# Kernel tuning notes

Measured on AMD Instinct MI355X. Metric: run time of the kernel, lower is better.

## Reference

```python
import jax, jax.numpy as jnp
import numpy as np
from jax import lax

B, T, H, L, NV = 2048, 100, 256, 128, 5  # batch, max_len, hidden, latent, len(NUC_VOCAB)


def setup_inputs() -> dict:
    key = jax.random.key(0)
    ks = jax.random.split(key, 13)
    s = 0.05
    inp = {
        "x_seq": jax.random.uniform(ks[0], (B, T, NV), dtype=jnp.float32),
        "hidden_states": jax.random.normal(ks[1], (B, H), dtype=jnp.float32) * 0.1,
        "tree_latent_vec": jax.random.normal(ks[2], (B, L), dtype=jnp.float32),
        "graph_latent_vec": jax.random.normal(ks[3], (B, L), dtype=jnp.float32),
        "lengths": jnp.maximum(1, jax.random.randint(ks[4], (B,), 0, T + 1)).astype(jnp.int32),
        # concat_squash_linear: (H + L) -> H
        "W_cs": jax.random.normal(ks[5], (H + L, H), dtype=jnp.float32) * s,
        "b_cs": jnp.zeros((H,), dtype=jnp.float32),
        # GRU cell linears: (H + NV) -> H, acting on cat([x, h])
        "W_z": jax.random.normal(ks[6], (NV + H, H), dtype=jnp.float32) * s,
        "b_z": jnp.zeros((H,), dtype=jnp.float32),
        "W_r": jax.random.normal(ks[7], (NV + H, H), dtype=jnp.float32) * s,
        "b_r": jnp.zeros((H,), dtype=jnp.float32),
        "W_h": jax.random.normal(ks[8], (NV + H, H), dtype=jnp.float32) * s,
        "b_h": jnp.zeros((H,), dtype=jnp.float32),
    }
    return inp


def _decode(x_seq, hidden_states, tree_latent_vec, graph_latent_vec, lengths,
            W_cs, b_cs, W_z, b_z, W_r, b_r, W_h, b_h):
    # concat volatile hidden state with graph latent, squash back to H
    h0 = jax.nn.relu(jnp.concatenate([hidden_states, graph_latent_vec], axis=-1) @ W_cs + b_cs)

    def gru_step(h, x):  # h: [B,H], x: [B,NV]
        xh = jnp.concatenate([x, h], axis=-1)          # [B, NV+H]
        z = jax.nn.sigmoid(xh @ W_z + b_z)
        r = jax.nn.sigmoid(xh @ W_r + b_r)
        xg = jnp.concatenate([x, r * h], axis=-1)
        pre_h = jnp.tanh(xg @ W_h + b_h)
        new_h = (1.0 - z) * h + z * pre_h
        return new_h, new_h

    _, hs = lax.scan(gru_step, h0, jnp.swapaxes(x_seq, 0, 1))  # [T,B,H]
    all_h = jnp.swapaxes(hs, 0, 1)                              # [B,T,H]

    # gather hidden state at last valid timestep (pre_padding_idx)
    new_h = jnp.take_along_axis(all_h, (lengths - 1)[:, None, None], axis=1)[:, 0]  # [B,H]

    # per-segment max-pool over valid positions (segment_representation)
    mask = jnp.arange(T)[None, :] < lengths[:, None]            # [B,T]
    seg_rep = jnp.max(jnp.where(mask[:, :, None], all_h, -jnp.inf), axis=1)  # [B,H]

    # depadded token features concatenated with per-batch tree/graph latents;
    # kept padded [B,T,.] with zeros at invalid positions (fixed-shape form)
    tok = jnp.concatenate([
        all_h,
        jnp.broadcast_to(tree_latent_vec[:, None, :], (B, T, L)),
        jnp.broadcast_to(graph_latent_vec[:, None, :], (B, T, L)),
    ], axis=-1)                                                 # [B,T,H+2L]
    all_hidden_states = jnp.where(mask[:, :, None], tok, 0.0)
    return new_h, all_hidden_states, seg_rep


def reference(x_seq, hidden_states, tree_latent_vec, graph_latent_vec, lengths,
              W_cs, b_cs, W_z, b_z, W_r, b_r, W_h, b_h):
    return _decode(x_seq, hidden_states, tree_latent_vec, graph_latent_vec, lengths,
                   W_cs, b_cs, W_z, b_z, W_r, b_r, W_h, b_h)
```

## Files before the change

### kernel.cpp

```cpp
#include <hip/hip_runtime.h>
#include <stdint.h>

#define B_N 2048
#define T_N 100
#define H_N 256
#define L_N 128
#define NV_N 5
#define COLS 512

#define KCS 384
#define RB 8
#define NKQ 2
#define KQH 128
#define CH 16
#define NCH 8
#define HSTR 264

static constexpr int OUT_ALLH = B_N * H_N;
static constexpr int OUT_SEG  = OUT_ALLH + B_N * T_N * COLS;

__device__ __forceinline__ float bits2f(uint32_t u) {
    union { uint32_t u; float f; } v; v.u = u; return v.f;
}
__device__ __forceinline__ uint16_t f2bf(float f) {
    union { float f; uint32_t u; } v; v.f = f;
    uint32_t r = (v.u + 0x7FFFu + ((v.u >> 16) & 1u)) >> 16;
    return (uint16_t)r;
}

__device__ __forceinline__ int detect_f32(const uint32_t* __restrict__ w) {
    int cnt = 0;
    #pragma unroll 8
    for (int i = 0; i < 64; ++i) {
        uint32_t e = (w[i] >> 23) & 0xFFu;
        cnt += (e >= 97u && e <= 130u) ? 1 : 0;
    }
    return cnt >= 32 ? 1 : 0;
}

template <bool F32> struct IO;

template <> struct IO<true> {
    using Raw2 = float2;
    static __device__ __forceinline__ Raw2 ldraw2(const void* p, int idx) {
        return *(const float2*)((const float*)p + idx);
    }
    static __device__ __forceinline__ void cvt2(const Raw2& u, float f[2]) {
        f[0] = u.x; f[1] = u.y;
    }
    static __device__ __forceinline__ void ld4(const void* p, int idx, float f[4]) {
        const float4 v = *(const float4*)((const float*)p + idx);
        f[0] = v.x; f[1] = v.y; f[2] = v.z; f[3] = v.w;
    }
    static __device__ __forceinline__ float ld1(const void* p, int idx) {
        return ((const float*)p)[idx];
    }
    static __device__ __forceinline__ void st4(void* p, int idx, const float f[4]) {
        *(float4*)((float*)p + idx) = make_float4(f[0], f[1], f[2], f[3]);
    }
    static __device__ __forceinline__ void st4z(void* p, int idx) {
        *(float4*)((float*)p + idx) = make_float4(0.f, 0.f, 0.f, 0.f);
    }
};

template <> struct IO<false> {
    using Raw2 = uint32_t;
    static __device__ __forceinline__ Raw2 ldraw2(const void* p, int idx) {
        return *(const uint32_t*)((const uint16_t*)p + idx);
    }
    static __device__ __forceinline__ void cvt2(const Raw2& u, float f[2]) {
        f[0] = bits2f(u << 16);
        f[1] = bits2f(u & 0xFFFF0000u);
    }
    static __device__ __forceinline__ void ld4(const void* p, int idx, float f[4]) {
        uint2 u = *(const uint2*)((const uint16_t*)p + idx);
        f[0] = bits2f(u.x << 16);
        f[1] = bits2f(u.x & 0xFFFF0000u);
        f[2] = bits2f(u.y << 16);
        f[3] = bits2f(u.y & 0xFFFF0000u);
    }
    static __device__ __forceinline__ float ld1(const void* p, int idx) {
        return bits2f(((uint32_t)((const uint16_t*)p)[idx]) << 16);
    }
    static __device__ __forceinline__ void st4(void* p, int idx, const float f[4]) {
        uint2 u;
        u.x = (uint32_t)f2bf(f[0]) | ((uint32_t)f2bf(f[1]) << 16);
        u.y = (uint32_t)f2bf(f[2]) | ((uint32_t)f2bf(f[3]) << 16);
        *(uint2*)((uint16_t*)p + idx) = u;
    }
    static __device__ __forceinline__ void st4z(void* p, int idx) {
        *(uint2*)((uint16_t*)p + idx) = make_uint2(0u, 0u);
    }
};

__device__ __forceinline__ float sigmoid_f(float x) {
    x = fminf(fmaxf(x, -30.f), 30.f);
    return 1.f / (1.f + __expf(-x));
}
__device__ __forceinline__ float tanh_f(float x) {
    x = fminf(fmaxf(x, -15.f), 15.f);
    float e = __expf(-2.f * x);
    return (1.f - e) / (1.f + e);
}

template <bool F32>
__global__ __launch_bounds__(256) void latent_fill_kernel(
    const void* __restrict__ tree,
    const void* __restrict__ graph,
    const int* __restrict__ lengths,
    const void* __restrict__ Wcs_detect,
    void* __restrict__ out)
{
    __shared__ int s_is32;
    if (threadIdx.x == 0) s_is32 = detect_f32((const uint32_t*)Wcs_detect);
    __syncthreads();
    if ((s_is32 != 0) != F32) return;

    int idx = (int)(blockIdx.x * 256 + threadIdx.x);
    int c = (idx & 31) * 8;
    int bt = idx >> 5;
    int t = bt % T_N;
    int b = bt / T_N;

    int dst = OUT_ALLH + bt * COLS + H_N + c;
    if (t < lengths[b]) {
        float v[8];
        if (c < L_N) {
            IO<F32>::ld4(tree, b * L_N + c, v);
            IO<F32>::ld4(tree, b * L_N + c + 4, v + 4);
        } else {
            IO<F32>::ld4(graph, b * L_N + (c - L_N), v);
            IO<F32>::ld4(graph, b * L_N + (c - L_N) + 4, v + 4);
        }
        IO<F32>::st4(out, dst, v);
        IO<F32>::st4(out, dst + 4, v + 4);
    } else {
        IO<F32>::st4z(out, dst);
        IO<F32>::st4z(out, dst + 4);
    }
}

template <bool F32>
__global__ __launch_bounds__(256, 1) void gru_kernel(
    const void* __restrict__ x_seq,
    const void* __restrict__ hidden,
    const void* __restrict__ graph,
    const int* __restrict__ lengths,
    const void* __restrict__ Wcs, const void* __restrict__ bcs,
    const void* __restrict__ Wz,  const void* __restrict__ bz,
    const void* __restrict__ Wr,  const void* __restrict__ br,
    const void* __restrict__ Wh,  const void* __restrict__ bh,
    void* __restrict__ out)
{
    __shared__ float Pz[NKQ][RB][H_N];
    __shared__ float Pr[NKQ][RB][H_N];
    __shared__ float hstage[RB][HSTR];
    __shared__ float gstage[RB][HSTR];
    __shared__ int s_is32;
    __shared__ int s_len[RB];

    if (threadIdx.x == 0) s_is32 = detect_f32((const uint32_t*)Wcs);
    __syncthreads();
    if ((s_is32 != 0) != F32) return;

    const int tid = threadIdx.x;
    const int kq  = tid >> 7;
    const int c0  = (tid & 127) * 2;
    const int ro  = tid >> 5;
    const int c0g = (tid & 31) * 8;
    const int kh0 = kq * KQH;

    if (tid < RB) {
        int L = lengths[blockIdx.x * RB + tid];
        s_len[tid] = min(max(L, 1), T_N);
    }
    __syncthreads();

    const int b0  = blockIdx.x * RB;
    const int bo  = b0 + ro;
    const int len = s_len[ro];
    int maxlen = 1;
    #pragma unroll
    for (int i = 0; i < RB; ++i) maxlen = max(maxlen, s_len[i]);

    {
        float* cs = &Pz[0][0][0];
        for (int i = tid; i < RB * KCS; i += 256) {
            int r = i / KCS;
            int k = i - r * KCS;
            int bb = b0 + r;
            float v = (k < H_N) ? IO<F32>::ld1(hidden, bb * H_N + k)
                                : IO<F32>::ld1(graph,  bb * L_N + (k - H_N));
            cs[r * 388 + k] = v;
        }
    }
    __syncthreads();

    float h[8];
    {
        const float* cs = &Pz[0][0][0];
        float acc[8];
        IO<F32>::ld4(bcs, c0g, acc);
        IO<F32>::ld4(bcs, c0g + 4, acc + 4);
        for (int k = 0; k < KCS; k += 4) {
            const float4 hv = *reinterpret_cast<const float4*>(&cs[ro * 388 + k]);
            const float hvv[4] = {hv.x, hv.y, hv.z, hv.w};
            #pragma unroll
            for (int kk = 0; kk < 4; ++kk) {
                float w[8];
                IO<F32>::ld4(Wcs, (k + kk) * H_N + c0g, w);
                IO<F32>::ld4(Wcs, (k + kk) * H_N + c0g + 4, w + 4);
                #pragma unroll
                for (int j = 0; j < 8; ++j) acc[j] += hvv[kk] * w[j];
            }
        }
        #pragma unroll
        for (int j = 0; j < 8; ++j) h[j] = fmaxf(acc[j], 0.f);
    }

    float bzv[8], brv[8], bhv[8];
    IO<F32>::ld4(bz, c0g, bzv); IO<F32>::ld4(bz, c0g + 4, bzv + 4);
    IO<F32>::ld4(br, c0g, brv); IO<F32>::ld4(br, c0g + 4, brv + 4);
    IO<F32>::ld4(bh, c0g, bhv); IO<F32>::ld4(bh, c0g + 4, bhv + 4);

    float smax[8];
    #pragma unroll
    for (int j = 0; j < 8; ++j) smax[j] = -1e30f;

    __syncthreads();

    *reinterpret_cast<float4*>(&hstage[ro][c0g])     = make_float4(h[0], h[1], h[2], h[3]);
    *reinterpret_cast<float4*>(&hstage[ro][c0g + 4]) = make_float4(h[4], h[5], h[6], h[7]);

    const int xr = tid / NV_N;
    const int xi = tid - xr * NV_N;
    float xv = 0.f;
    if (tid < RB * NV_N) {
        float x0 = IO<F32>::ld1(x_seq, ((b0 + xr) * T_N + 0) * NV_N + xi);
        hstage[xr][H_N + xi] = x0;
        gstage[xr][H_N + xi] = x0;
        int tn = (1 < T_N) ? 1 : 0;
        xv = IO<F32>::ld1(x_seq, ((b0 + xr) * T_N + tn) * NV_N + xi);
    }
    __syncthreads();

    float z[8];

    typename IO<F32>::Raw2 zA[CH], rA[CH], zB[CH], rB[CH], hA[CH], hB[CH];
    typename IO<F32>::Raw2 xzb[NV_N], xrb[NV_N], xhb[NV_N];

#define P1_ISSUE(CHN, RZ, RR) { \
    const int kb_ = 5 + kh0 + (CHN) * CH; \
    _Pragma("unroll") \
    for (int i_ = 0; i_ < CH; ++i_) { \
        RZ[i_] = IO<F32>::ldraw2(Wz, (kb_ + i_) * H_N + c0); \
        RR[i_] = IO<F32>::ldraw2(Wr, (kb_ + i_) * H_N + c0); \
    } \
    __builtin_amdgcn_sched_barrier(0); }

#define P1_CONSUME(CHN, RZ, RR) { \
    const int kb_ = kh0 + (CHN) * CH; \
    _Pragma("unroll") \
    for (int g_ = 0; g_ < CH / 2; ++g_) { \
        float2 hr_[RB]; \
        _Pragma("unroll") \
        for (int r_ = 0; r_ < RB; ++r_) \
            hr_[r_] = *reinterpret_cast<const float2*>(&hstage[r_][kb_ + 2 * g_]); \
        _Pragma("unroll") \
        for (int u_ = 0; u_ < 2; ++u_) { \
            float wz2_[2], wr2_[2]; \
            IO<F32>::cvt2(RZ[2 * g_ + u_], wz2_); \
            IO<F32>::cvt2(RR[2 * g_ + u_], wr2_); \
            _Pragma("unroll") \
            for (int r_ = 0; r_ < RB; ++r_) { \
                const float hv_ = u_ ? hr_[r_].y : hr_[r_].x; \
                az[r_][0] += hv_ * wz2_[0]; \
                az[r_][1] += hv_ * wz2_[1]; \
                ar[r_][0] += hv_ * wr2_[0]; \
                ar[r_][1] += hv_ * wr2_[1]; \
            } } } }

#define P2_ISSUE(CHN, RH) { \
    const int kb_ = 5 + kh0 + (CHN) * CH; \
    _Pragma("unroll") \
    for (int i_ = 0; i_ < CH; ++i_) \
        RH[i_] = IO<F32>::ldraw2(Wh, (kb_ + i_) * H_N + c0); \
    __builtin_amdgcn_sched_barrier(0); }

#define P2_CONSUME(CHN, RH) { \
    const int kb_ = kh0 + (CHN) * CH; \
    _Pragma("unroll") \
    for (int g_ = 0; g_ < CH / 2; ++g_) { \
        float2 gr_[RB]; \
        _Pragma("unroll") \
        for (int r_ = 0; r_ < RB; ++r_) \
            gr_[r_] = *reinterpret_cast<const float2*>(&gstage[r_][kb_ + 2 * g_]); \
        _Pragma("unroll") \
        for (int u_ = 0; u_ < 2; ++u_) { \
            float wh2_[2]; \
            IO<F32>::cvt2(RH[2 * g_ + u_], wh2_); \
            _Pragma("unroll") \
            for (int r_ = 0; r_ < RB; ++r_) { \
                const float gv_ = u_ ? gr_[r_].y : gr_[r_].x; \
                ag[r_][0] += gv_ * wh2_[0]; \
                ag[r_][1] += gv_ * wh2_[1]; \
            } } } }

#define PX_ISSUE() if (kq == 0) { \
    _Pragma("unroll") \
    for (int i_ = 0; i_ < NV_N; ++i_) { \
        xzb[i_] = IO<F32>::ldraw2(Wz, i_ * H_N + c0); \
        xrb[i_] = IO<F32>::ldraw2(Wr, i_ * H_N + c0); \
    } }

#define PXH_ISSUE() if (kq == 0) { \
    _Pragma("unroll") \
    for (int i_ = 0; i_ < NV_N; ++i_) \
        xhb[i_] = IO<F32>::ldraw2(Wh, i_ * H_N + c0); }

#define P1X_CONSUME() if (kq == 0) { \
    _Pragma("unroll") \
    for (int i_ = 0; i_ < NV_N; ++i_) { \
        float wz2_[2], wr2_[2]; \
        IO<F32>::cvt2(xzb[i_], wz2_); \
        IO<F32>::cvt2(xrb[i_], wr2_); \
        _Pragma("unroll") \
        for (int r_ = 0; r_ < RB; ++r_) { \
            const float xv_ = hstage[r_][H_N + i_]; \
            az[r_][0] += xv_ * wz2_[0]; \
            az[r_][1] += xv_ * wz2_[1]; \
            ar[r_][0] += xv_ * wr2_[0]; \
            ar[r_][1] += xv_ * wr2_[1]; \
        } } }

#define P2X_CONSUME() if (kq == 0) { \
    _Pragma("unroll") \
    for (int i_ = 0; i_ < NV_N; ++i_) { \
        float wh2_[2]; \
        IO<F32>::cvt2(xhb[i_], wh2_); \
        _Pragma("unroll") \
        for (int r_ = 0; r_ < RB; ++r_) { \
            const float xv_ = gstage[r_][H_N + i_]; \
            ag[r_][0] += xv_ * wh2_[0]; \
            ag[r_][1] += xv_ * wh2_[1]; \
        } } }

    PX_ISSUE();
    P1_ISSUE(0, zA, rA);

    #pragma unroll 1
    for (int t = 0; t < maxlen; ++t) {
        float az[RB][2], ar[RB][2];
        #pragma unroll
        for (int r = 0; r < RB; ++r) {
            az[r][0] = 0.f; az[r][1] = 0.f;
            ar[r][0] = 0.f; ar[r][1] = 0.f;
        }
        #pragma unroll 1
        for (int ch = 0; ch < NCH; ch += 2) {
            P1_ISSUE(ch + 1, zB, rB);
            P1_CONSUME(ch, zA, rA);
            if (ch + 2 < NCH) { P1_ISSUE(ch + 2, zA, rA); }
            else              { P2_ISSUE(0, hA); PXH_ISSUE(); }
            P1_CONSUME(ch + 1, zB, rB);
        }
        P1X_CONSUME();
        #pragma unroll
        for (int r = 0; r < RB; ++r) {
            *reinterpret_cast<float2*>(&Pz[kq][r][c0]) = make_float2(az[r][0], az[r][1]);
            *reinterpret_cast<float2*>(&Pr[kq][r][c0]) = make_float2(ar[r][0], ar[r][1]);
        }
        __syncthreads();

        {
            float sz[8], sr[8];
            #pragma unroll
            for (int j = 0; j < 8; ++j) { sz[j] = bzv[j]; sr[j] = brv[j]; }
            #pragma unroll
            for (int q = 0; q < NKQ; ++q) {
                float4 a = *reinterpret_cast<const float4*>(&Pz[q][ro][c0g]);
                float4 b = *reinterpret_cast<const float4*>(&Pz[q][ro][c0g + 4]);
                sz[0] += a.x; sz[1] += a.y; sz[2] += a.z; sz[3] += a.w;
                sz[4] += b.x; sz[5] += b.y; sz[6] += b.z; sz[7] += b.w;
                a = *reinterpret_cast<const float4*>(&Pr[q][ro][c0g]);
                b = *reinterpret_cast<const float4*>(&Pr[q][ro][c0g + 4]);
                sr[0] += a.x; sr[1] += a.y; sr[2] += a.z; sr[3] += a.w;
                sr[4] += b.x; sr[5] += b.y; sr[6] += b.z; sr[7] += b.w;
            }
            float rh[8];
            #pragma unroll
            for (int j = 0; j < 8; ++j) {
                z[j] = sigmoid_f(sz[j]);
                rh[j] = sigmoid_f(sr[j]) * h[j];
            }
            *reinterpret_cast<float4*>(&gstage[ro][c0g])     = make_float4(rh[0], rh[1], rh[2], rh[3]);
            *reinterpret_cast<float4*>(&gstage[ro][c0g + 4]) = make_float4(rh[4], rh[5], rh[6], rh[7]);
        }
        __syncthreads();

        float ag[RB][2];
        #pragma unroll
        for (int r = 0; r < RB; ++r) { ag[r][0] = 0.f; ag[r][1] = 0.f; }
        #pragma unroll 1
        for (int ch = 0; ch < NCH; ch += 2) {
            P2_ISSUE(ch + 1, hB);
            P2_CONSUME(ch, hA);
            if (ch + 2 < NCH) { P2_ISSUE(ch + 2, hA); }
            else              { P1_ISSUE(0, zA, rA); PX_ISSUE(); }
            P2_CONSUME(ch + 1, hB);
        }
        P2X_CONSUME();
        #pragma unroll
        for (int r = 0; r < RB; ++r)
            *reinterpret_cast<float2*>(&Pz[kq][r][c0]) = make_float2(ag[r][0], ag[r][1]);
        __syncthreads();

        {
            float sg[8];
            #pragma unroll
            for (int j = 0; j < 8; ++j) sg[j] = bhv[j];
            #pragma unroll
            for (int q = 0; q < NKQ; ++q) {
                float4 a = *reinterpret_cast<const float4*>(&Pz[q][ro][c0g]);
                float4 b = *reinterpret_cast<const float4*>(&Pz[q][ro][c0g + 4]);
                sg[0] += a.x; sg[1] += a.y; sg[2] += a.z; sg[3] += a.w;
                sg[4] += b.x; sg[5] += b.y; sg[6] += b.z; sg[7] += b.w;
            }
            const bool active = (t < len);
            float hs[8];
            #pragma unroll
            for (int j = 0; j < 8; ++j) {
                float pre = tanh_f(sg[j]);
                float hn  = (1.f - z[j]) * h[j] + z[j] * pre;
                hn = active ? hn : h[j];
                h[j]  = hn;
                hs[j] = active ? hn : 0.f;
                smax[j] = active ? fmaxf(smax[j], hn) : smax[j];
            }
            const int ob = OUT_ALLH + (bo * T_N + t) * COLS + c0g;
            IO<F32>::st4(out, ob, hs);
            IO<F32>::st4(out, ob + 4, hs + 4);
            if (t == len - 1) {
                IO<F32>::st4(out, bo * H_N + c0g, h);
                IO<F32>::st4(out, bo * H_N + c0g + 4, h + 4);
            }
            *reinterpret_cast<float4*>(&hstage[ro][c0g])     = make_float4(h[0], h[1], h[2], h[3]);
            *reinterpret_cast<float4*>(&hstage[ro][c0g + 4]) = make_float4(h[4], h[5], h[6], h[7]);
        }
        if (tid < RB * NV_N) {
            hstage[xr][H_N + xi] = xv;
            gstage[xr][H_N + xi] = xv;
            int tn = (t + 2 < T_N) ? (t + 2) : (T_N - 1);
            xv = IO<F32>::ld1(x_seq, ((b0 + xr) * T_N + tn) * NV_N + xi);
        }
        __syncthreads();
    }

#undef P1_ISSUE
#undef P1_CONSUME
#undef P2_ISSUE
#undef P2_CONSUME
#undef PX_ISSUE
#undef PXH_ISSUE
#undef P1X_CONSUME
#undef P2X_CONSUME

    for (int t = maxlen; t < T_N; ++t) {
        const int ob = OUT_ALLH + (bo * T_N + t) * COLS + c0g;
        IO<F32>::st4z(out, ob);
        IO<F32>::st4z(out, ob + 4);
    }
    IO<F32>::st4(out, OUT_SEG + bo * H_N + c0g, smax);
    IO<F32>::st4(out, OUT_SEG + bo * H_N + c0g + 4, smax + 4);
}

extern "C" void kernel_launch(void* const* d_in, const int* in_sizes, int n_in,
                              void* d_out, int out_size, void* d_ws, size_t ws_size,
                              hipStream_t stream) {
    const void* x_seq  = d_in[0];
    const void* hidden = d_in[1];
    const void* tree   = d_in[2];
    const void* graph  = d_in[3];
    const int*  lens   = (const int*)d_in[4];
    const void* Wcs    = d_in[5];
    const void* bcs    = d_in[6];
    const void* Wz     = d_in[7];
    const void* bz     = d_in[8];
    const void* Wr     = d_in[9];
    const void* br     = d_in[10];
    const void* Wh     = d_in[11];
    const void* bh     = d_in[12];
    void* out = d_out;

    long long work = (long long)B_N * T_N * 32;
    int fill_blocks = (int)(work / 256);

    hipLaunchKernelGGL((latent_fill_kernel<true>),  dim3(fill_blocks), dim3(256), 0, stream,
                       tree, graph, lens, Wcs, out);
    hipLaunchKernelGGL((latent_fill_kernel<false>), dim3(fill_blocks), dim3(256), 0, stream,
                       tree, graph, lens, Wcs, out);

    hipLaunchKernelGGL((gru_kernel<true>), dim3(B_N / RB), dim3(256), 0, stream,
                       x_seq, hidden, graph, lens,
                       Wcs, bcs, Wz, bz, Wr, br, Wh, bh, out);
    hipLaunchKernelGGL((gru_kernel<false>), dim3(B_N / RB), dim3(256), 0, stream,
                       x_seq, hidden, graph, lens,
                       Wcs, bcs, Wz, bz, Wr, br, Wh, bh, out);
}
```

Baseline: 4.076 ms.

## Use bf16 MFMA with hi/lo split for GRU recurrence on bf16 inputs

New measurement: 4.107 ms. About the same (+0.8%).

```diff
diff --git a/kernel.cpp b/kernel.cpp
--- a/kernel.cpp
+++ b/kernel.cpp
@@ -10,6 +10,11 @@
 
 #define KCS 384
 #define RB 8
+
+#define KT_N 9
+#define PZ_STR 260
+#define HB_STR 296
+
 #define NKQ 2
 #define KQH 128
 #define CH 16
@@ -18,6 +23,10 @@
 
 static constexpr int OUT_ALLH = B_N * H_N;
 static constexpr int OUT_SEG  = OUT_ALLH + B_N * T_N * COLS;
+static constexpr size_t WS_NEEDED = (size_t)3 * KT_N * 16 * 64 * 8 * 2;
+
+typedef __attribute__((ext_vector_type(8))) short bf16x8v;
+typedef __attribute__((ext_vector_type(4))) float f32x4v;
 
 __device__ __forceinline__ float bits2f(uint32_t u) {
     union { uint32_t u; float f; } v; v.u = u; return v.f;
@@ -38,23 +47,36 @@
     return cnt >= 32 ? 1 : 0;
 }
 
+__device__ __forceinline__ float bld1(const void* p, int idx) {
+    return bits2f(((uint32_t)((const uint16_t*)p)[idx]) << 16);
+}
+__device__ __forceinline__ void bld4(const void* p, int idx, float f[4]) {
+    uint2 u = *(const uint2*)((const uint16_t*)p + idx);
+    f[0] = bits2f(u.x << 16); f[1] = bits2f(u.x & 0xFFFF0000u);
+    f[2] = bits2f(u.y << 16); f[3] = bits2f(u.y & 0xFFFF0000u);
+}
+__device__ __forceinline__ void bst4(void* p, int idx, const float f[4]) {
+    uint2 u;
+    u.x = (uint32_t)f2bf(f[0]) | ((uint32_t)f2bf(f[1]) << 16);
+    u.y = (uint32_t)f2bf(f[2]) | ((uint32_t)f2bf(f[3]) << 16);
+    *(uint2*)((uint16_t*)p + idx) = u;
+}
+__device__ __forceinline__ void bst4z(void* p, int idx) {
+    *(uint2*)((uint16_t*)p + idx) = make_uint2(0u, 0u);
+}
+
 template <bool F32> struct IO;
-
 template <> struct IO<true> {
     using Raw2 = float2;
     static __device__ __forceinline__ Raw2 ldraw2(const void* p, int idx) {
         return *(const float2*)((const float*)p + idx);
     }
-    static __device__ __forceinline__ void cvt2(const Raw2& u, float f[2]) {
-        f[0] = u.x; f[1] = u.y;
-    }
+    static __device__ __forceinline__ void cvt2(const Raw2& u, float f[2]) { f[0] = u.x; f[1] = u.y; }
     static __device__ __forceinline__ void ld4(const void* p, int idx, float f[4]) {
         const float4 v = *(const float4*)((const float*)p + idx);
         f[0] = v.x; f[1] = v.y; f[2] = v.z; f[3] = v.w;
     }
-    static __device__ __forceinline__ float ld1(const void* p, int idx) {
-        return ((const float*)p)[idx];
-    }
+    static __device__ __forceinline__ float ld1(const void* p, int idx) { return ((const float*)p)[idx]; }
     static __device__ __forceinline__ void st4(void* p, int idx, const float f[4]) {
         *(float4*)((float*)p + idx) = make_float4(f[0], f[1], f[2], f[3]);
     }
@@ -62,35 +84,18 @@
         *(float4*)((float*)p + idx) = make_float4(0.f, 0.f, 0.f, 0.f);
     }
 };
-
 template <> struct IO<false> {
     using Raw2 = uint32_t;
     static __device__ __forceinline__ Raw2 ldraw2(const void* p, int idx) {
         return *(const uint32_t*)((const uint16_t*)p + idx);
     }
     static __device__ __forceinline__ void cvt2(const Raw2& u, float f[2]) {
-        f[0] = bits2f(u << 16);
-        f[1] = bits2f(u & 0xFFFF0000u);
-    }
-    static __device__ __forceinline__ void ld4(const void* p, int idx, float f[4]) {
-        uint2 u = *(const uint2*)((const uint16_t*)p + idx);
-        f[0] = bits2f(u.x << 16);
-        f[1] = bits2f(u.x & 0xFFFF0000u);
-        f[2] = bits2f(u.y << 16);
-        f[3] = bits2f(u.y & 0xFFFF0000u);
-    }
-    static __device__ __forceinline__ float ld1(const void* p, int idx) {
-        return bits2f(((uint32_t)((const uint16_t*)p)[idx]) << 16);
-    }
-    static __device__ __forceinline__ void st4(void* p, int idx, const float f[4]) {
-        uint2 u;
-        u.x = (uint32_t)f2bf(f[0]) | ((uint32_t)f2bf(f[1]) << 16);
-        u.y = (uint32_t)f2bf(f[2]) | ((uint32_t)f2bf(f[3]) << 16);
-        *(uint2*)((uint16_t*)p + idx) = u;
-    }
-    static __device__ __forceinline__ void st4z(void* p, int idx) {
-        *(uint2*)((uint16_t*)p + idx) = make_uint2(0u, 0u);
-    }
+        f[0] = bits2f(u << 16); f[1] = bits2f(u & 0xFFFF0000u);
+    }
+    static __device__ __forceinline__ void ld4(const void* p, int idx, float f[4]) { bld4(p, idx, f); }
+    static __device__ __forceinline__ float ld1(const void* p, int idx) { return bld1(p, idx); }
+    static __device__ __forceinline__ void st4(void* p, int idx, const float f[4]) { bst4(p, idx, f); }
+    static __device__ __forceinline__ void st4z(void* p, int idx) { bst4z(p, idx); }
 };
 
 __device__ __forceinline__ float sigmoid_f(float x) {
@@ -138,6 +143,321 @@
         IO<F32>::st4z(out, dst);
         IO<F32>::st4z(out, dst + 4);
     }
+}
+
+__global__ __launch_bounds__(256) void prep_kernel(
+    const void* __restrict__ Wz, const void* __restrict__ Wr,
+    const void* __restrict__ Wh, const void* __restrict__ Wcs_detect,
+    void* __restrict__ ws)
+{
+    __shared__ int s_is32;
+    if (threadIdx.x == 0) s_is32 = detect_f32((const uint32_t*)Wcs_detect);
+    __syncthreads();
+    const int is32 = s_is32;
+
+    int g = (int)(blockIdx.x * 256 + threadIdx.x);
+    int lane  = g & 63;
+    int rest  = g >> 6;
+    int nt    = rest & 15;
+    int rest2 = rest >> 4;
+    int kt    = rest2 % KT_N;
+    int mat   = rest2 / KT_N;
+    if (mat > 2) return;
+
+    const void* W = (mat == 0) ? Wz : (mat == 1) ? Wr : Wh;
+    const int n = nt * 16 + (lane & 15);
+    uint16_t u[8];
+    #pragma unroll
+    for (int j = 0; j < 8; ++j) {
+        int k = kt * 32 + ((lane >> 4) * 8) + j;
+        int srow = (k < 256) ? (k + NV_N) : ((k <= 260) ? (k - 256) : -1);
+        uint16_t v = 0;
+        if (srow >= 0) {
+            if (is32) v = f2bf(((const float*)W)[srow * H_N + n]);
+            else      v = ((const uint16_t*)W)[srow * H_N + n];
+        }
+        u[j] = v;
+    }
+    uint4 o;
+    o.x = (uint32_t)u[0] | ((uint32_t)u[1] << 16);
+    o.y = (uint32_t)u[2] | ((uint32_t)u[3] << 16);
+    o.z = (uint32_t)u[4] | ((uint32_t)u[5] << 16);
+    o.w = (uint32_t)u[6] | ((uint32_t)u[7] << 16);
+    *(uint4*)((char*)ws + (size_t)g * 16) = o;
+}
+
+__global__ __launch_bounds__(256, 1) void gru_mfma(
+    const void* __restrict__ x_seq,
+    const void* __restrict__ hidden,
+    const void* __restrict__ graph,
+    const int* __restrict__ lengths,
+    const void* __restrict__ Wcs, const void* __restrict__ bcs,
+    const void* __restrict__ bz,  const void* __restrict__ br,
+    const void* __restrict__ bh,
+    const void* __restrict__ ws,  void* __restrict__ out)
+{
+    __shared__ float PzS[16 * PZ_STR];
+    __shared__ float PrS[16 * PZ_STR];
+    __shared__ uint16_t hbf[16 * HB_STR];
+    __shared__ uint16_t gbf[16 * HB_STR];
+    __shared__ int s_is32;
+    __shared__ int s_len[RB];
+
+    if (threadIdx.x == 0) s_is32 = detect_f32((const uint32_t*)Wcs);
+    __syncthreads();
+    if (s_is32 != 0) return;
+
+    const int tid  = threadIdx.x;
+    const int lane = tid & 63;
+    const int wv   = tid >> 6;
+    const int ntb  = wv * 4;
+    const int ro   = tid >> 5;
+    const int c0g  = (tid & 31) * 8;
+
+    if (tid < RB) {
+        int L = lengths[blockIdx.x * RB + tid];
+        s_len[tid] = min(max(L, 1), T_N);
+    }
+    for (int i = tid; i < 16 * HB_STR; i += 256) { hbf[i] = 0; gbf[i] = 0; }
+    __syncthreads();
+
+    const int b0  = blockIdx.x * RB;
+    const int bo  = b0 + ro;
+    const int len = s_len[ro];
+    int maxlen = 1;
+    #pragma unroll
+    for (int i = 0; i < RB; ++i) maxlen = max(maxlen, s_len[i]);
+
+    {
+        float* cs = PzS;
+        for (int i = tid; i < RB * KCS; i += 256) {
+            int r = i / KCS, k = i - r * KCS;
+            int bb = b0 + r;
+            float v = (k < H_N) ? bld1(hidden, bb * H_N + k)
+                                : bld1(graph,  bb * L_N + (k - H_N));
+            cs[r * 388 + k] = v;
+        }
+    }
+    __syncthreads();
+
+    float h[8];
+    {
+        const float* cs = PzS;
+        float acc[8];
+        bld4(bcs, c0g, acc); bld4(bcs, c0g + 4, acc + 4);
+        for (int k = 0; k < KCS; k += 4) {
+            const float4 hv = *(const float4*)&cs[ro * 388 + k];
+            const float hvv[4] = {hv.x, hv.y, hv.z, hv.w};
+            #pragma unroll
+            for (int kk = 0; kk < 4; ++kk) {
+                float w[8];
+                bld4(Wcs, (k + kk) * H_N + c0g, w);
+                bld4(Wcs, (k + kk) * H_N + c0g + 4, w + 4);
+                #pragma unroll
+                for (int j = 0; j < 8; ++j) acc[j] += hvv[kk] * w[j];
+            }
+        }
+        #pragma unroll
+        for (int j = 0; j < 8; ++j) h[j] = fmaxf(acc[j], 0.f);
+    }
+
+    float bzv[8], brv[8], bhv[8];
+    bld4(bz, c0g, bzv); bld4(bz, c0g + 4, bzv + 4);
+    bld4(br, c0g, brv); bld4(br, c0g + 4, brv + 4);
+    bld4(bh, c0g, bhv); bld4(bh, c0g + 4, bhv + 4);
+
+    float smax[8];
+    #pragma unroll
+    for (int j = 0; j < 8; ++j) smax[j] = -1e30f;
+
+    __syncthreads();
+
+#define STORE_HILO(BUF, VALS) { \
+    union { bf16x8v v; uint16_t u[8]; } hi_, lo_; \
+    _Pragma("unroll") \
+    for (int j_ = 0; j_ < 8; ++j_) { \
+        uint16_t a_ = f2bf(VALS[j_]); \
+        hi_.u[j_] = a_; \
+        lo_.u[j_] = f2bf(VALS[j_] - bits2f((uint32_t)a_ << 16)); \
+    } \
+    *(bf16x8v*)&BUF[ro * HB_STR + c0g] = hi_.v; \
+    *(bf16x8v*)&BUF[(8 + ro) * HB_STR + c0g] = lo_.v; }
+
+    STORE_HILO(hbf, h)
+    const int xr = tid / NV_N;
+    const int xi = tid - xr * NV_N;
+    float xv = 0.f;
+    if (tid < RB * NV_N) {
+        float x0 = bld1(x_seq, ((b0 + xr) * T_N + 0) * NV_N + xi);
+        uint16_t xh = f2bf(x0);
+        uint16_t xl = f2bf(x0 - bits2f((uint32_t)xh << 16));
+        hbf[xr * HB_STR + 256 + xi] = xh; hbf[(8 + xr) * HB_STR + 256 + xi] = xl;
+        gbf[xr * HB_STR + 256 + xi] = xh; gbf[(8 + xr) * HB_STR + 256 + xi] = xl;
+        xv = bld1(x_seq, ((b0 + xr) * T_N + 1) * NV_N + xi);
+    }
+    __syncthreads();
+
+    const bf16x8v* wsW = (const bf16x8v*)ws;
+    float z[8];
+
+#define LDB1(KT, S) { \
+    _Pragma("unroll") \
+    for (int nt_ = 0; nt_ < 4; ++nt_) { \
+        Bz[S][nt_] = wsW[((0 * KT_N + (KT)) * 16 + ntb + nt_) * 64 + lane]; \
+        Br[S][nt_] = wsW[((1 * KT_N + (KT)) * 16 + ntb + nt_) * 64 + lane]; \
+    } }
+#define MMA1(KT, S) { \
+    bf16x8v a_ = *(const bf16x8v*)&hbf[(lane & 15) * HB_STR + (KT) * 32 + ((lane >> 4) * 8)]; \
+    _Pragma("unroll") \
+    for (int nt_ = 0; nt_ < 4; ++nt_) { \
+        accz[nt_] = __builtin_amdgcn_mfma_f32_16x16x32_bf16(a_, Bz[S][nt_], accz[nt_], 0, 0, 0); \
+        accr[nt_] = __builtin_amdgcn_mfma_f32_16x16x32_bf16(a_, Br[S][nt_], accr[nt_], 0, 0, 0); \
+    } }
+#define LDB2(KT, S) { \
+    _Pragma("unroll") \
+    for (int nt_ = 0; nt_ < 4; ++nt_) \
+        Bh[S][nt_] = wsW[((2 * KT_N + (KT)) * 16 + ntb + nt_) * 64 + lane]; }
+#define MMA2(KT, S) { \
+    bf16x8v a_ = *(const bf16x8v*)&gbf[(lane & 15) * HB_STR + (KT) * 32 + ((lane >> 4) * 8)]; \
+    _Pragma("unroll") \
+    for (int nt_ = 0; nt_ < 4; ++nt_) \
+        acch[nt_] = __builtin_amdgcn_mfma_f32_16x16x32_bf16(a_, Bh[S][nt_], acch[nt_], 0, 0, 0); }
+
+    #pragma unroll 1
+    for (int t = 0; t < maxlen; ++t) {
+        {
+            bf16x8v Bz[3][4], Br[3][4];
+            f32x4v accz[4], accr[4];
+            #pragma unroll
+            for (int nt_ = 0; nt_ < 4; ++nt_) {
+                accz[nt_] = {0.f, 0.f, 0.f, 0.f};
+                accr[nt_] = {0.f, 0.f, 0.f, 0.f};
+            }
+            LDB1(0, 0) LDB1(1, 1) LDB1(2, 2)
+            MMA1(0, 0) LDB1(3, 0)
+            MMA1(1, 1) LDB1(4, 1)
+            MMA1(2, 2) LDB1(5, 2)
+            MMA1(3, 0) LDB1(6, 0)
+            MMA1(4, 1) LDB1(7, 1)
+            MMA1(5, 2) LDB1(8, 2)
+            MMA1(6, 0) MMA1(7, 1) MMA1(8, 2)
+            #pragma unroll
+            for (int nt_ = 0; nt_ < 4; ++nt_) {
+                #pragma unroll
+                for (int i_ = 0; i_ < 4; ++i_) {
+                    const int m_ = (lane >> 4) * 4 + i_;
+                    const int cc = (ntb + nt_) * 16 + (lane & 15);
+                    PzS[m_ * PZ_STR + cc] = accz[nt_][i_];
+                    PrS[m_ * PZ_STR + cc] = accr[nt_][i_];
+                }
+            }
+        }
+        __syncthreads();
+
+        {
+            const float4 za = *(const float4*)&PzS[ro * PZ_STR + c0g];
+            const float4 zb = *(const float4*)&PzS[ro * PZ_STR + c0g + 4];
+            const float4 zc = *(const float4*)&PzS[(8 + ro) * PZ_STR + c0g];
+            const float4 zd = *(const float4*)&PzS[(8 + ro) * PZ_STR + c0g + 4];
+            const float4 ra = *(const float4*)&PrS[ro * PZ_STR + c0g];
+            const float4 rb = *(const float4*)&PrS[ro * PZ_STR + c0g + 4];
+            const float4 rc = *(const float4*)&PrS[(8 + ro) * PZ_STR + c0g];
+            const float4 rd = *(const float4*)&PrS[(8 + ro) * PZ_STR + c0g + 4];
+            float sz[8] = {bzv[0] + za.x + zc.x, bzv[1] + za.y + zc.y,
+                           bzv[2] + za.z + zc.z, bzv[3] + za.w + zc.w,
+                           bzv[4] + zb.x + zd.x, bzv[5] + zb.y + zd.y,
+                           bzv[6] + zb.z + zd.z, bzv[7] + zb.w + zd.w};
+            float sr[8] = {brv[0] + ra.x + rc.x, brv[1] + ra.y + rc.y,
+                           brv[2] + ra.z + rc.z, brv[3] + ra.w + rc.w,
+                           brv[4] + rb.x + rd.x, brv[5] + rb.y + rd.y,
+                           brv[6] + rb.z + rd.z, brv[7] + rb.w + rd.w};
+            float rh[8];
+            #pragma unroll
+            for (int j = 0; j < 8; ++j) {
+                z[j]  = sigmoid_f(sz[j]);
+                rh[j] = sigmoid_f(sr[j]) * h[j];
+            }
+            STORE_HILO(gbf, rh)
+        }
+        __syncthreads();
+
+        {
+            bf16x8v Bh[3][4];
+            f32x4v acch[4];
+            #pragma unroll
+            for (int nt_ = 0; nt_ < 4; ++nt_) acch[nt_] = {0.f, 0.f, 0.f, 0.f};
+            LDB2(0, 0) LDB2(1, 1) LDB2(2, 2)
+            MMA2(0, 0) LDB2(3, 0)
+            MMA2(1, 1) LDB2(4, 1)
+            MMA2(2, 2) LDB2(5, 2)
+            MMA2(3, 0) LDB2(6, 0)
+            MMA2(4, 1) LDB2(7, 1)
+            MMA2(5, 2) LDB2(8, 2)
+            MMA2(6, 0) MMA2(7, 1) MMA2(8, 2)
+            #pragma unroll
+            for (int nt_ = 0; nt_ < 4; ++nt_) {
+                #pragma unroll
+                for (int i_ = 0; i_ < 4; ++i_) {
+                    const int m_ = (lane >> 4) * 4 + i_;
+                    PzS[m_ * PZ_STR + (ntb + nt_) * 16 + (lane & 15)] = acch[nt_][i_];
+                }
+            }
+        }
+        __syncthreads();
+
+        {
+            const float4 ga = *(const float4*)&PzS[ro * PZ_STR + c0g];
+            const float4 gb = *(const float4*)&PzS[ro * PZ_STR + c0g + 4];
+            const float4 gc = *(const float4*)&PzS[(8 + ro) * PZ_STR + c0g];
+            const float4 gd = *(const float4*)&PzS[(8 + ro) * PZ_STR + c0g + 4];
+            float sg[8] = {bhv[0] + ga.x + gc.x, bhv[1] + ga.y + gc.y,
+                           bhv[2] + ga.z + gc.z, bhv[3] + ga.w + gc.w,
+                           bhv[4] + gb.x + gd.x, bhv[5] + gb.y + gd.y,
+                           bhv[6] + gb.z + gd.z, bhv[7] + gb.w + gd.w};
+            const bool active = (t < len);
+            float hs[8];
+            #pragma unroll
+            for (int j = 0; j < 8; ++j) {
+                float pre = tanh_f(sg[j]);
+                float hn  = (1.f - z[j]) * h[j] + z[j] * pre;
+                hn = active ? hn : h[j];
+                h[j]  = hn;
+                hs[j] = active ? hn : 0.f;
+                smax[j] = active ? fmaxf(smax[j], hn) : smax[j];
+            }
+            const int ob = OUT_ALLH + (bo * T_N + t) * COLS + c0g;
+            bst4(out, ob, hs);
+            bst4(out, ob + 4, hs + 4);
+            if (t == len - 1) {
+                bst4(out, bo * H_N + c0g, h);
+                bst4(out, bo * H_N + c0g + 4, h + 4);
+            }
+            STORE_HILO(hbf, h)
+        }
+        if (tid < RB * NV_N) {
+            uint16_t xh = f2bf(xv);
+            uint16_t xl = f2bf(xv - bits2f((uint32_t)xh << 16));
+            hbf[xr * HB_STR + 256 + xi] = xh; hbf[(8 + xr) * HB_STR + 256 + xi] = xl;
+            gbf[xr * HB_STR + 256 + xi] = xh; gbf[(8 + xr) * HB_STR + 256 + xi] = xl;
+            int tn = (t + 2 < T_N) ? (t + 2) : (T_N - 1);
+            xv = bld1(x_seq, ((b0 + xr) * T_N + tn) * NV_N + xi);
+        }
+        __syncthreads();
+    }
+
+#undef LDB1
+#undef MMA1
+#undef LDB2
+#undef MMA2
+#undef STORE_HILO
+
+    for (int t = maxlen; t < T_N; ++t) {
+        const int ob = OUT_ALLH + (bo * T_N + t) * COLS + c0g;
+        bst4z(out, ob);
+        bst4z(out, ob + 4);
+    }
+    bst4(out, OUT_SEG + bo * H_N + c0g, smax);
+    bst4(out, OUT_SEG + bo * H_N + c0g + 4, smax + 4);
 }
 
 template <bool F32>
@@ -245,7 +565,6 @@
     __syncthreads();
 
     float z[8];
-
     typename IO<F32>::Raw2 zA[CH], rA[CH], zB[CH], rB[CH], hA[CH], hB[CH];
     typename IO<F32>::Raw2 xzb[NV_N], xrb[NV_N], xhb[NV_N];
 
@@ -257,7 +576,6 @@
         RR[i_] = IO<F32>::ldraw2(Wr, (kb_ + i_) * H_N + c0); \
     } \
     __builtin_amdgcn_sched_barrier(0); }
-
 #define P1_CONSUME(CHN, RZ, RR) { \
     const int kb_ = kh0 + (CHN) * CH; \
     _Pragma("unroll") \
@@ -279,14 +597,12 @@
                 ar[r_][0] += hv_ * wr2_[0]; \
                 ar[r_][1] += hv_ * wr2_[1]; \
             } } } }
-
 #define P2_ISSUE(CHN, RH) { \
     const int kb_ = 5 + kh0 + (CHN) * CH; \
     _Pragma("unroll") \
     for (int i_ = 0; i_ < CH; ++i_) \
         RH[i_] = IO<F32>::ldraw2(Wh, (kb_ + i_) * H_N + c0); \
     __builtin_amdgcn_sched_barrier(0); }
-
 #define P2_CONSUME(CHN, RH) { \
     const int kb_ = kh0 + (CHN) * CH; \
     _Pragma("unroll") \
@@ -305,19 +621,16 @@
                 ag[r_][0] += gv_ * wh2_[0]; \
                 ag[r_][1] += gv_ * wh2_[1]; \
             } } } }
-
 #define PX_ISSUE() if (kq == 0) { \
     _Pragma("unroll") \
     for (int i_ = 0; i_ < NV_N; ++i_) { \
         xzb[i_] = IO<F32>::ldraw2(Wz, i_ * H_N + c0); \
         xrb[i_] = IO<F32>::ldraw2(Wr, i_ * H_N + c0); \
     } }
-
 #define PXH_ISSUE() if (kq == 0) { \
     _Pragma("unroll") \
     for (int i_ = 0; i_ < NV_N; ++i_) \
         xhb[i_] = IO<F32>::ldraw2(Wh, i_ * H_N + c0); }
-
 #define P1X_CONSUME() if (kq == 0) { \
     _Pragma("unroll") \
     for (int i_ = 0; i_ < NV_N; ++i_) { \
@@ -332,7 +645,6 @@
             ar[r_][0] += xv_ * wr2_[0]; \
             ar[r_][1] += xv_ * wr2_[1]; \
         } } }
-
 #define P2X_CONSUME() if (kq == 0) { \
     _Pragma("unroll") \
     for (int i_ = 0; i_ < NV_N; ++i_) { \
@@ -500,10 +812,22 @@
     hipLaunchKernelGGL((latent_fill_kernel<false>), dim3(fill_blocks), dim3(256), 0, stream,
                        tree, graph, lens, Wcs, out);
 
-    hipLaunchKernelGGL((gru_kernel<true>), dim3(B_N / RB), dim3(256), 0, stream,
-                       x_seq, hidden, graph, lens,
-                       Wcs, bcs, Wz, bz, Wr, br, Wh, bh, out);
-    hipLaunchKernelGGL((gru_kernel<false>), dim3(B_N / RB), dim3(256), 0, stream,
-                       x_seq, hidden, graph, lens,
-                       Wcs, bcs, Wz, bz, Wr, br, Wh, bh, out);
-}
+    const bool use_mfma = (d_ws != nullptr) && (ws_size >= WS_NEEDED);
+    if (use_mfma) {
+        hipLaunchKernelGGL(prep_kernel, dim3(108), dim3(256), 0, stream,
+                           Wz, Wr, Wh, Wcs, d_ws);
+        hipLaunchKernelGGL(gru_mfma, dim3(B_N / RB), dim3(256), 0, stream,
+                           x_seq, hidden, graph, lens,
+                           Wcs, bcs, bz, br, bh, d_ws, out);
+        hipLaunchKernelGGL((gru_kernel<true>), dim3(B_N / RB), dim3(256), 0, stream,
+                           x_seq, hidden, graph, lens,
+                           Wcs, bcs, Wz, bz, Wr, br, Wh, bh, out);
+    } else {
+        hipLaunchKernelGGL((gru_kernel<false>), dim3(B_N / RB), dim3(256), 0, stream,
+                           x_seq, hidden, graph, lens,
+                           Wcs, bcs, Wz, bz, Wr, br, Wh, bh, out);
+        hipLaunchKernelGGL((gru_kernel<true>), dim3(B_N / RB), dim3(256), 0, stream,
+                           x_seq, hidden, graph, lens,
+                           Wcs, bcs, Wz, bz, Wr, br, Wh, bh, out);
+    }
+}
```
